# Kernel tuning notes

Measured on AMD Instinct MI355X. Metric: run time of the kernel, lower is better.

The kernel has to match this reference:

```python
import jax, jax.numpy as jnp
import numpy as np
from jax import lax

N_FT = 1024          # Fourier grid size (module default n_ft)
X_RANGE = 0.3        # module default x_range: data rescaled into torus
TWO_PI = 2.0 * np.pi


def gaussian_sliced_kernel_ft(h, d, sigma_sq):
    """Fourier coefficients of the 1D basis function whose slicing gives the
    d-dim Gaussian kernel exp(-r^2/(2 sigma^2)):
        khat(h) = (2 pi^2 sigma^2)^(d/2) |h|^(d-1) exp(-2 pi^2 sigma^2 h^2) / Gamma(d/2)
    Computed in log-space for numerical stability (|h|^(d-1) overflows for d=64).
    """
    habs = jnp.abs(h)
    logv = (0.5 * d) * jnp.log(2.0 * np.pi ** 2 * sigma_sq) \
        + (d - 1.0) * jnp.log(jnp.where(habs > 0, habs, 1.0)) \
        - 2.0 * np.pi ** 2 * sigma_sq * h ** 2 \
        - lax.lgamma(jnp.asarray(d / 2.0, dtype=jnp.float32))
    return jnp.where(habs > 0, jnp.exp(logv), 0.0).astype(jnp.float32)


def setup_inputs():
    key = jax.random.key(0)
    k1, k2, k3, k4 = jax.random.split(key, 4)
    N, M, d, P = 8192, 8192, 64, 64
    x = jax.random.normal(k1, (N, d), dtype=jnp.float32)
    y = jax.random.normal(k2, (M, d), dtype=jnp.float32)
    x_weights = jax.random.normal(k3, (N,), dtype=jnp.float32)
    xis = jax.random.normal(k4, (P, d), dtype=jnp.float32)
    xis = xis / jnp.linalg.norm(xis, axis=-1, keepdims=True)  # unit slice directions
    scale = jnp.ones((1,), dtype=jnp.float32)
    return {"x": x, "y": y, "x_weights": x_weights, "scale": scale, "xis": xis}


def reference(x, y, x_weights, scale, xis):
    # Sliced fast Gaussian kernel summation:
    #   out(y_m) = (1/P) sum_p sum_n w_n k1d(<xi_p, x_n - y_m>)
    # where the 1D convolution per slice is evaluated through its Fourier series
    # (the exact NDFT sum that the module's NFFT approximates).
    d = x.shape[1]
    scale_s = jnp.reshape(scale, ())
    # precomputation: rescale data so all points fit in the torus window
    norm_max = jnp.maximum(jnp.max(jnp.linalg.norm(x, axis=-1)),
                           jnp.max(jnp.linalg.norm(y, axis=-1)))
    sf = X_RANGE / norm_max
    xs, ys = x * sf, y * sf
    scale_r = scale_s * sf
    h = jnp.arange(-(N_FT // 2), N_FT // 2, dtype=jnp.float32)  # (K,) frequencies
    kft = gaussian_sliced_kernel_ft(h, d, scale_r ** 2)          # (K,) real, symmetric
    w = x_weights.astype(jnp.complex64)

    def one_slice(acc, xi):
        a = xs @ xi  # (N,) projected source points
        b = ys @ xi  # (M,) projected target points
        # adjoint NDFT: yhat_k = sum_n w_n exp(2 pi i h_k a_n)
        yhat = jnp.exp(1j * TWO_PI * h[:, None] * a[None, :]) @ w        # (K,)
        # forward NDFT at targets: s_m = sum_k kft_k * yhat_k * exp(-2 pi i h_k b_m)
        s = jnp.exp(-1j * TWO_PI * b[:, None] * h[None, :]) @ (kft * yhat)  # (M,)
        return acc + s.real.astype(jnp.float32), None

    acc0 = jnp.zeros(y.shape[0], dtype=jnp.float32)
    total, _ = lax.scan(one_slice, acc0, xis)  # sequential over slices = batch_size_P
    return total / xis.shape[0]
```

## Files before the change

### kernel.cpp

```cpp
#include <hip/hip_runtime.h>
#include <math.h>

#define N_SRC 8192
#define D_DIM 64
#define P_SL  64
#define KH    512

#define WS_NM    0
#define WS_CS    16
#define WS_A     (WS_CS + P_SL*KH*2)
#define WS_B2    (WS_A + P_SL*N_SRC)

#define LOG_THRESH (-23.0259f)
#define LGAMMA32    78.0922236f
#define TWO_PI2     19.7392088f

__device__ __forceinline__ void sincos2pi(float t, float& s, float& c) {
    float f = __builtin_amdgcn_fractf(t);
    s = __builtin_amdgcn_sinf(f);
    c = __builtin_amdgcn_cosf(f);
}

__global__ __launch_bounds__(256) void kA(const float* __restrict__ x,
                                          const float* __restrict__ y,
                                          const float* __restrict__ xis,
                                          float* __restrict__ ws,
                                          float* __restrict__ out) {
    int tid = threadIdx.x, b = blockIdx.x;
    int rblk = b & 63, q = b >> 6;
    int r = rblk * 256 + tid;
    int isx = (r < N_SRC);
    const float* src = isx ? (x + (size_t)r * D_DIM)
                           : (y + (size_t)(r - N_SRC) * D_DIM);
    float4 row[16];
    const float4* rp = (const float4*)src;
#pragma unroll
    for (int j = 0; j < 16; ++j) row[j] = rp[j];

    if (q == 0) {
        float ss = 0.f;
#pragma unroll
        for (int j = 0; j < 16; ++j) {
            ss = fmaf(row[j].x, row[j].x, ss); ss = fmaf(row[j].y, row[j].y, ss);
            ss = fmaf(row[j].z, row[j].z, ss); ss = fmaf(row[j].w, row[j].w, ss);
        }
        float nm = sqrtf(ss);
        for (int o = 32; o; o >>= 1) nm = fmaxf(nm, __shfl_xor(nm, o, 64));
        if ((tid & 63) == 0)
            atomicMax((int*)ws + WS_NM, __float_as_int(nm));
    }

    int gtid = b * 256 + tid;
    if (gtid < P_SL * KH * 2) ws[WS_CS + gtid] = 0.f;
    if (gtid < N_SRC)         out[gtid] = 0.f;

    int rr = isx ? r : r - N_SRC;
    float* dst = ws + (isx ? WS_A : WS_B2);
    for (int pi = 0; pi < 8; ++pi) {
        int p = q * 8 + pi;
        const float4* xi = (const float4*)(xis + p * D_DIM);
        float acc = 0.f;
#pragma unroll
        for (int j = 0; j < 16; ++j) {
            float4 u = xi[j];
            acc = fmaf(row[j].x, u.x, acc); acc = fmaf(row[j].y, u.y, acc);
            acc = fmaf(row[j].z, u.z, acc); acc = fmaf(row[j].w, u.w, acc);
        }
        dst[(size_t)p * N_SRC + rr] = acc;
    }
}

__global__ __launch_bounds__(256) void kB(const float* __restrict__ xw,
                                          const float* __restrict__ scale,
                                          float* __restrict__ ws) {
    __shared__ int skmin, skmax;
    __shared__ float sC[64], sS[64];
    int tid = threadIdx.x;
    int chunk = blockIdx.x, p = blockIdx.y;
    if (tid == 0) { skmin = 0x7fffffff; skmax = 0; }
    __syncthreads();
    float nm = __int_as_float(((const int*)ws)[WS_NM]);
    float sf = 0.3f / nm;
    float sr = scale[0] * sf;
    float a = TWO_PI2 * sr * sr;
    float la = logf(a);
    for (int k = tid + 1; k <= KH; k += 256) {
        float logv = 32.f * la + 63.f * logf((float)k)
                   - a * (float)k * (float)k - LGAMMA32;
        if (logv > LOG_THRESH) { atomicMin(&skmin, k); atomicMax(&skmax, k); }
    }
    __syncthreads();
    int kmin = skmin, kmax = skmax;
    if (kmax == 0) return;
    int kcnt = kmax - kmin + 1;
    int lane = tid & 63;
    int wv = __builtin_amdgcn_readfirstlane(tid >> 6);
    const float* ap = ws + WS_A + (size_t)p * N_SRC + chunk * 512 + wv * 128;
    const float* wp = xw + chunk * 512 + wv * 128;
    for (int kbase = 0; kbase < kcnt; kbase += 64) {
        __syncthreads();
        if (tid < 64) { sC[tid] = 0.f; sS[tid] = 0.f; }
        __syncthreads();
        float fk = (float)(kmin + kbase + lane) * sf;
        float ca = 0.f, sa = 0.f;
#pragma unroll 8
        for (int j = 0; j < 128; ++j) {
            float aj = ap[j], wj = wp[j];
            float t = fk * aj;
            float s, c; sincos2pi(t, s, c);
            ca = fmaf(wj, c, ca);
            sa = fmaf(wj, s, sa);
        }
        atomicAdd(&sC[lane], ca);
        atomicAdd(&sS[lane], sa);
        __syncthreads();
        int ki = kbase + tid;
        if (tid < 64 && ki < kcnt) {
            int kk = kmin + ki;
            float logv = 32.f * la + 63.f * logf((float)kk)
                       - a * (float)kk * (float)kk - LGAMMA32;
            float wk = ((kk == KH) ? 1.f : 2.f) * expf(logv) * (1.f / (float)P_SL);
            atomicAdd(ws + WS_CS + ((size_t)p * KH + ki) * 2 + 0, wk * sC[tid]);
            atomicAdd(ws + WS_CS + ((size_t)p * KH + ki) * 2 + 1, wk * sS[tid]);
        }
    }
}

__global__ __launch_bounds__(256) void kC(const float* __restrict__ scale,
                                          float* __restrict__ ws,
                                          float* __restrict__ out) {
    __shared__ int skmin, skmax;
    int tid = threadIdx.x;
    if (tid == 0) { skmin = 0x7fffffff; skmax = 0; }
    __syncthreads();
    float nm = __int_as_float(((const int*)ws)[WS_NM]);
    float sf = 0.3f / nm;
    float sr = scale[0] * sf;
    float a = TWO_PI2 * sr * sr;
    float la = logf(a);
    for (int k = tid + 1; k <= KH; k += 256) {
        float logv = 32.f * la + 63.f * logf((float)k)
                   - a * (float)k * (float)k - LGAMMA32;
        if (logv > LOG_THRESH) { atomicMin(&skmin, k); atomicMax(&skmax, k); }
    }
    __syncthreads();
    int kmin = skmin, kmax = skmax;
    if (kmax == 0) return;
    int kcnt = kmax - kmin + 1;
    int m = blockIdx.x * 256 + tid;
    int pg = blockIdx.y;
    float sum = 0.f;
    for (int pi = 0; pi < 4; ++pi) {
        int p = pg * 4 + pi;
        float bm = ws[WS_B2 + (size_t)p * N_SRC + m] * sf;
        const float2* cs = (const float2*)(ws + WS_CS) + (size_t)p * KH;
#pragma unroll 4
        for (int i = 0; i < kcnt; ++i) {
            float2 q = cs[i];
            float t = bm * (float)(kmin + i);
            float s, c; sincos2pi(t, s, c);
            sum = fmaf(q.x, c, sum);
            sum = fmaf(q.y, s, sum);
        }
    }
    atomicAdd(out + m, sum);
}

extern "C" void kernel_launch(void* const* d_in, const int* in_sizes, int n_in,
                              void* d_out, int out_size, void* d_ws, size_t ws_size,
                              hipStream_t stream) {
    const float* x     = (const float*)d_in[0];
    const float* y     = (const float*)d_in[1];
    const float* xw    = (const float*)d_in[2];
    const float* scale = (const float*)d_in[3];
    const float* xis   = (const float*)d_in[4];
    float* ws  = (float*)d_ws;
    float* out = (float*)d_out;

    kA<<<dim3(512),      dim3(256), 0, stream>>>(x, y, xis, ws, out);
    kB<<<dim3(16, 64),   dim3(256), 0, stream>>>(xw, scale, ws);
    kC<<<dim3(32, 16),   dim3(256), 0, stream>>>(scale, ws, out);
}
```

Before: 107.8 us.

## Replace per-frequency sincos with angle-addition recurrences in adjoint and forward NDFT

Both NDFT kernels now evaluate one sincos per point and per block of frequencies, then step through neighbouring frequencies with complex rotation recurrences instead of calling sin/cos for every (point, frequency) pair. In kB each thread now holds 4 source points and builds 64 frequency accumulators, which are reduced across the wave with a butterfly shuffle transpose; the grid is halved to 8 chunks of 1024 points. The aim is to cut transcendental instruction count. The cost is higher register pressure from the 64-entry accumulator arrays, and rounding error that builds up over 8 or 16 recurrence steps.

```diff
diff --git a/kernel.cpp b/kernel.cpp
--- a/kernel.cpp
+++ b/kernel.cpp
@@ -94,26 +94,66 @@
     if (kmax == 0) return;
     int kcnt = kmax - kmin + 1;
     int lane = tid & 63;
-    int wv = __builtin_amdgcn_readfirstlane(tid >> 6);
-    const float* ap = ws + WS_A + (size_t)p * N_SRC + chunk * 512 + wv * 128;
-    const float* wp = xw + chunk * 512 + wv * 128;
+
+    int base = chunk * 1024 + tid;
+    const float* ap = ws + WS_A + (size_t)p * N_SRC;
+    float pa_[4], pw_[4], th_[4], rc_[4], rs_[4];
+#pragma unroll
+    for (int j = 0; j < 4; ++j) {
+        pa_[j] = ap[base + 256 * j];
+        pw_[j] = xw[base + 256 * j];
+        th_[j] = pa_[j] * sf;
+        sincos2pi(th_[j], rs_[j], rc_[j]);
+    }
+
     for (int kbase = 0; kbase < kcnt; kbase += 64) {
         __syncthreads();
         if (tid < 64) { sC[tid] = 0.f; sS[tid] = 0.f; }
         __syncthreads();
-        float fk = (float)(kmin + kbase + lane) * sf;
-        float ca = 0.f, sa = 0.f;
-#pragma unroll 8
-        for (int j = 0; j < 128; ++j) {
-            float aj = ap[j], wj = wp[j];
-            float t = fk * aj;
-            float s, c; sincos2pi(t, s, c);
-            ca = fmaf(wj, c, ca);
-            sa = fmaf(wj, s, sa);
-        }
-        atomicAdd(&sC[lane], ca);
-        atomicAdd(&sS[lane], sa);
+
+        float accC[64], accS[64];
+        float pc_[4], ps_[4];
+#pragma unroll
+        for (int blk = 0; blk < 4; ++blk) {
+            float f0 = (float)(kmin + kbase + blk * 16);
+#pragma unroll
+            for (int j = 0; j < 4; ++j) {
+                float t0 = th_[j] * f0;
+                float ss0, cc0; sincos2pi(t0, ss0, cc0);
+                pc_[j] = cc0 * pw_[j];
+                ps_[j] = ss0 * pw_[j];
+            }
+#pragma unroll
+            for (int u = 0; u < 16; ++u) {
+                int i = blk * 16 + u;
+                accC[i] = (pc_[0] + pc_[1]) + (pc_[2] + pc_[3]);
+                accS[i] = (ps_[0] + ps_[1]) + (ps_[2] + ps_[3]);
+#pragma unroll
+                for (int j = 0; j < 4; ++j) {
+                    float nc = fmaf(pc_[j], rc_[j], -(ps_[j] * rs_[j]));
+                    float ns = fmaf(ps_[j], rc_[j],  pc_[j] * rs_[j]);
+                    pc_[j] = nc; ps_[j] = ns;
+                }
+            }
+        }
+
+#pragma unroll
+        for (int h = 32; h >= 1; h >>= 1) {
+            bool hb = (lane & h) != 0;
+#pragma unroll
+            for (int i = 0; i < h; ++i) {
+                float sc = hb ? accC[i]     : accC[i + h];
+                float ssv = hb ? accS[i]     : accS[i + h];
+                float kc = hb ? accC[i + h] : accC[i];
+                float ks = hb ? accS[i + h] : accS[i];
+                accC[i] = kc + __shfl_xor(sc, h, 64);
+                accS[i] = ks + __shfl_xor(ssv, h, 64);
+            }
+        }
+        atomicAdd(&sC[lane], accC[0]);
+        atomicAdd(&sS[lane], accS[0]);
         __syncthreads();
+
         int ki = kbase + tid;
         if (tid < 64 && ki < kcnt) {
             int kk = kmin + ki;
@@ -154,13 +194,22 @@
         int p = pg * 4 + pi;
         float bm = ws[WS_B2 + (size_t)p * N_SRC + m] * sf;
         const float2* cs = (const float2*)(ws + WS_CS) + (size_t)p * KH;
-#pragma unroll 4
-        for (int i = 0; i < kcnt; ++i) {
-            float2 q = cs[i];
-            float t = bm * (float)(kmin + i);
-            float s, c; sincos2pi(t, s, c);
-            sum = fmaf(q.x, c, sum);
-            sum = fmaf(q.y, s, sum);
+        float cr, crs; sincos2pi(bm, crs, cr);
+        for (int ib = 0; ib < kcnt; ib += 8) {
+            float t0 = bm * (float)(kmin + ib);
+            float c, s; sincos2pi(t0, s, c);
+#pragma unroll
+            for (int u = 0; u < 8; ++u) {
+                int i = ib + u;
+                if (i < kcnt) {
+                    float2 q = cs[i];
+                    sum = fmaf(q.x, c, sum);
+                    sum = fmaf(q.y, s, sum);
+                }
+                float nc = fmaf(c, cr, -(s * crs));
+                s = fmaf(s, cr, c * crs);
+                c = nc;
+            }
         }
     }
     atomicAdd(out + m, sum);
@@ -178,6 +227,6 @@
     float* out = (float*)d_out;
 
     kA<<<dim3(512),      dim3(256), 0, stream>>>(x, y, xis, ws, out);
-    kB<<<dim3(16, 64),   dim3(256), 0, stream>>>(xw, scale, ws);
+    kB<<<dim3(8, 64),    dim3(256), 0, stream>>>(xw, scale, ws);
     kC<<<dim3(32, 16),   dim3(256), 0, stream>>>(scale, ws, out);
 }
```

Result: no change. 108.2 us (+0.4%).
